# Optimization experiments

Measured on AMD Instinct MI355X. Metric: run time of the kernel, lower is better.

## Reference

```python
import jax, jax.numpy as jnp
import numpy as np

N = 50000          # nodes
E = 800000         # edges (avg degree 16)
H, D = 4, 32       # heads, per-head channels; hidden = H*D = 128
DIMS_IN = [32, 128, 128]


def setup_inputs() -> dict:
    key = jax.random.key(0)
    ks = jax.random.split(key, 40)
    inp = {}
    inp["x"] = jax.random.normal(ks[0], (N, 32), jnp.float32)
    inp["edge_index"] = jax.random.randint(ks[1], (2, E), 0, N, dtype=jnp.int32)
    i = 2
    for l, din in enumerate(DIMS_IN):
        for nm in ["q", "k", "v", "s"]:
            inp[f"W{nm}{l}"] = jax.random.normal(ks[i], (din, H * D), jnp.float32) / np.float32(np.sqrt(din)); i += 1
            inp[f"b{nm}{l}"] = jax.random.normal(ks[i], (H * D,), jnp.float32) * 0.01; i += 1
    inp["Wf"] = jax.random.normal(ks[i], (H * D, 1), jnp.float32) / np.float32(np.sqrt(H * D)); i += 1
    inp["bf"] = jax.random.normal(ks[i], (1,), jnp.float32) * 0.01
    return inp


def _transformer_conv(x, src, dst, Wq, bq, Wk, bk, Wv, bv, Ws, bs):
    """PyG TransformerConv (concat=True, root_weight=True, beta=False, eval mode)."""
    n = x.shape[0]
    q = (x @ Wq + bq).reshape(n, H, D)   # queries at nodes
    k = (x @ Wk + bk).reshape(n, H, D)
    v = (x @ Wv + bv).reshape(n, H, D)
    # per-edge attention score: q at destination, k at source
    s = jnp.einsum("ehd,ehd->eh", q[dst], k[src]) / np.float32(np.sqrt(D))  # [E,H]
    # segment softmax over incoming edges of each destination node
    m = jax.ops.segment_max(s, dst, num_segments=n)          # [N,H]
    e = jnp.exp(s - m[dst])                                  # [E,H]
    den = jax.ops.segment_sum(e, dst, num_segments=n)        # [N,H]
    alpha = e / den[dst]                                     # [E,H]
    agg = jax.ops.segment_sum(alpha[:, :, None] * v[src], dst, num_segments=n)  # [N,H,D]
    return agg.reshape(n, H * D) + (x @ Ws + bs)             # skip connection


def reference(x, edge_index,
              Wq0, bq0, Wk0, bk0, Wv0, bv0, Ws0, bs0,
              Wq1, bq1, Wk1, bk1, Wv1, bv1, Ws1, bs1,
              Wq2, bq2, Wk2, bk2, Wv2, bv2, Ws2, bs2,
              Wf, bf):
    src, dst = edge_index[0], edge_index[1]
    layers = [
        (Wq0, bq0, Wk0, bk0, Wv0, bv0, Ws0, bs0),
        (Wq1, bq1, Wk1, bk1, Wv1, bv1, Ws1, bs1),
        (Wq2, bq2, Wk2, bk2, Wv2, bv2, Ws2, bs2),
    ]
    h = x
    for p in layers:
        h = jax.nn.relu(_transformer_conv(h, src, dst, *p))
    out = jax.nn.sigmoid(h @ Wf + bf)  # [N,1]
    return out
```

## Files before the change

kernel.cpp:

```cpp
#include <hip/hip_runtime.h>
#include <hip/hip_bf16.h>
#include <cstdint>
#include <cstddef>

typedef __attribute__((ext_vector_type(8))) short bf16x8;
typedef __attribute__((ext_vector_type(4))) float f32x4;

__device__ __forceinline__ unsigned short f2bs(float f){
  __hip_bfloat16 h = __float2bfloat16(f);
  return *(unsigned short*)&h;
}
__device__ __forceinline__ float bflo(unsigned int u){ return __uint_as_float(u << 16); }
__device__ __forceinline__ float bfhi(unsigned int u){ return __uint_as_float(u & 0xffff0000u); }

__global__ void zero_int_kernel(int* __restrict__ p, int n){
  int i = blockIdx.x*256 + threadIdx.x;
  if (i < n) p[i] = 0;
}

__global__ void hist_kernel(const int* __restrict__ dst, int E, int* __restrict__ deg){
  int e = blockIdx.x*256 + threadIdx.x;
  if (e < E) atomicAdd(&deg[dst[e]], 1);
}

__global__ __launch_bounds__(1024)
void scanA_kernel(const int* __restrict__ deg, int n, int* __restrict__ rowptr, int* __restrict__ bsums){
  __shared__ int s[1024];
  int t = threadIdx.x;
  int i = blockIdx.x*1024 + t;
  int v = (i < n) ? deg[i] : 0;
  s[t] = v;
  __syncthreads();
  #pragma unroll
  for (int off = 1; off < 1024; off <<= 1){
    int a = (t >= off) ? s[t-off] : 0;
    __syncthreads();
    s[t] += a;
    __syncthreads();
  }
  if (i < n) rowptr[i] = s[t] - v;
  if (t == 1023) bsums[blockIdx.x] = s[1023];
}

__global__ void scanB_kernel(const int* __restrict__ bsums, int nch, int* __restrict__ choff){
  int t = threadIdx.x;
  int v = (t < nch) ? bsums[t] : 0;
  int x = v;
  #pragma unroll
  for (int off = 1; off < 64; off <<= 1){
    int u = __shfl_up(x, off, 64);
    if (t >= off) x += u;
  }
  choff[t] = x - v;
}

__global__ __launch_bounds__(1024)
void scanC_kernel(const int* __restrict__ choff, int n, int* __restrict__ rowptr, int* __restrict__ cursor){
  int i = blockIdx.x*1024 + threadIdx.x;
  if (i < n){
    int r = rowptr[i] + choff[blockIdx.x];
    rowptr[i] = r;
    cursor[i] = r;
  }
}

__global__ void scatter_kernel(const int* __restrict__ src, const int* __restrict__ dst, int E,
                               int* __restrict__ cursor, int* __restrict__ adj){
  int e = blockIdx.x*256 + threadIdx.x;
  if (e < E){
    int pos = atomicAdd(&cursor[dst[e]], 1);
    adj[pos] = src[e];
  }
}

struct PrepArgs {
  const float* w[12];
  unsigned short* o[12];
};

__global__ void transpose_w_kernel(PrepArgs a){
  int m = blockIdx.y;
  int K = (m < 4) ? 32 : 128;
  int halfK = K >> 1;
  int tot = 128 * halfK;
  int e = blockIdx.x*256 + threadIdx.x;
  if (e >= tot) return;
  int n  = e / halfK;
  int k2 = e % halfK;
  const float* W = a.w[m];
  unsigned int lo = __float_as_uint(W[(2*k2)  *128 + n]) >> 16;
  unsigned int hi = __float_as_uint(W[(2*k2+1)*128 + n]) & 0xffff0000u;
  ((unsigned int*)a.o[m])[e] = lo | hi;
}

__global__ void cvt_x_kernel(const float* __restrict__ x, unsigned short* __restrict__ xb, int n2){
  int i = blockIdx.x*256 + threadIdx.x;
  if (i < n2){
    float2 v = ((const float2*)x)[i];
    ((unsigned int*)xb)[i] = (__float_as_uint(v.x) >> 16) | (__float_as_uint(v.y) & 0xffff0000u);
  }
}

template<int DIN>
__global__ __launch_bounds__(256)
void gemm4_mfma(const unsigned short* __restrict__ X, int nn,
                const unsigned short* __restrict__ T0, const unsigned short* __restrict__ T1,
                const unsigned short* __restrict__ T2, const unsigned short* __restrict__ T3,
                const float* __restrict__ b0, const float* __restrict__ b1,
                const float* __restrict__ b2, const float* __restrict__ b3,
                unsigned short* __restrict__ O0, unsigned short* __restrict__ O1,
                unsigned short* __restrict__ O2, unsigned short* __restrict__ O3)
{
  constexpr int KP = DIN + 8;
  __shared__ __align__(16) unsigned short wt[128*KP];
  int t = threadIdx.x;
  int msel = blockIdx.y;
  const unsigned short* WT = (msel==0)?T0:(msel==1)?T1:(msel==2)?T2:T3;
  const float* B = (msel==0)?b0:(msel==1)?b1:(msel==2)?b2:b3;
  unsigned short* O = (msel==0)?O0:(msel==1)?O1:(msel==2)?O2:O3;

  {
    const int NU = 128*DIN/8;
    for (int u = t; u < NU; u += 256){
      uint4 v = ((const uint4*)WT)[u];
      int n = u / (DIN/8), b = u % (DIN/8);
      *(uint4*)&wt[n*KP + b*8] = v;
    }
  }

  int lane = t & 63, wv = t >> 6;
  int m0 = blockIdx.x*64 + wv*16;
  int n16 = lane & 15, quad = lane >> 4;

  bf16x8 af[DIN/32];
  {
    const unsigned short* xrow = X + (size_t)(m0 + n16)*DIN + quad*8;
    #pragma unroll
    for (int s = 0; s < DIN/32; s++) af[s] = *(const bf16x8*)(xrow + s*32);
  }

  __syncthreads();

  f32x4 acc[8];
  #pragma unroll
  for (int c=0;c<8;c++) acc[c] = (f32x4){0.f,0.f,0.f,0.f};

  #pragma unroll
  for (int s = 0; s < DIN/32; s++){
    #pragma unroll
    for (int c = 0; c < 8; c++){
      bf16x8 bf = *(const bf16x8*)&wt[(c*16 + n16)*KP + s*32 + quad*8];
      acc[c] = __builtin_amdgcn_mfma_f32_16x16x32_bf16(af[s], bf, acc[c], 0, 0, 0);
    }
  }

  #pragma unroll
  for (int c = 0; c < 8; c++){
    int col = c*16 + n16;
    float bias = B[col];
    #pragma unroll
    for (int r = 0; r < 4; r++){
      int row = m0 + quad*4 + r;
      if (row < nn) O[(size_t)row*128 + col] = f2bs(acc[c][r] + bias);
    }
  }
}

__global__ __launch_bounds__(256)
void attn_kernel(const unsigned short* __restrict__ q,  const unsigned short* __restrict__ kmat,
                 const unsigned short* __restrict__ vmat, const unsigned short* __restrict__ skip,
                 const int* __restrict__ rowptr, const int* __restrict__ deg,
                 const int* __restrict__ adj, unsigned short* __restrict__ hout, int nn)
{
  int lane = threadIdx.x & 63, wid = threadIdx.x >> 6;
  int n = blockIdx.x*4 + wid;
  if (n >= nn) return;
  const float RS = 0.17677669529663687f;

  unsigned int qu = *(const unsigned int*)(q + (size_t)n*128 + 2*lane);
  float qx = bflo(qu), qy = bfhi(qu);
  int start = rowptr[n], dg = deg[n];
  float m = -INFINITY, l = 0.f, accx = 0.f, accy = 0.f;

  for (int c0 = 0; c0 < dg; c0 += 64){
    int cn = min(64, dg - c0);
    int idx = adj[start + c0 + min(lane, cn-1)];

    for (int g = 0; g < cn; g += 4){
      int gm = cn - g;
      int e1 = min(g+1, cn-1);
      int e2 = min(g+2, cn-1);
      int e3 = min(g+3, cn-1);
      int s0 = __shfl(idx, g , 64);
      int s1 = __shfl(idx, e1, 64);
      int s2 = __shfl(idx, e2, 64);
      int s3 = __shfl(idx, e3, 64);
      unsigned int ku0 = *(const unsigned int*)(kmat + (size_t)s0*128 + 2*lane);
      unsigned int ku1 = *(const unsigned int*)(kmat + (size_t)s1*128 + 2*lane);
      unsigned int ku2 = *(const unsigned int*)(kmat + (size_t)s2*128 + 2*lane);
      unsigned int ku3 = *(const unsigned int*)(kmat + (size_t)s3*128 + 2*lane);
      unsigned int vu0 = *(const unsigned int*)(vmat + (size_t)s0*128 + 2*lane);
      unsigned int vu1 = *(const unsigned int*)(vmat + (size_t)s1*128 + 2*lane);
      unsigned int vu2 = *(const unsigned int*)(vmat + (size_t)s2*128 + 2*lane);
      unsigned int vu3 = *(const unsigned int*)(vmat + (size_t)s3*128 + 2*lane);

      float p0 = qx*bflo(ku0) + qy*bfhi(ku0);
      float p1 = qx*bflo(ku1) + qy*bfhi(ku1);
      float p2 = qx*bflo(ku2) + qy*bfhi(ku2);
      float p3 = qx*bflo(ku3) + qy*bfhi(ku3);
      #pragma unroll
      for (int msk = 1; msk <= 8; msk <<= 1){
        p0 += __shfl_xor(p0, msk, 64);
        p1 += __shfl_xor(p1, msk, 64);
        p2 += __shfl_xor(p2, msk, 64);
        p3 += __shfl_xor(p3, msk, 64);
      }
      float f0 = p0*RS;
      float f1 = (gm > 1) ? p1*RS : -INFINITY;
      float f2 = (gm > 2) ? p2*RS : -INFINITY;
      float f3 = (gm > 3) ? p3*RS : -INFINITY;

      float gmax = fmaxf(fmaxf(f0,f1), fmaxf(f2,f3));
      float nm = fmaxf(m, gmax);
      float r  = __expf(m - nm);
      float w0 = __expf(f0 - nm);
      float w1 = __expf(f1 - nm);
      float w2 = __expf(f2 - nm);
      float w3 = __expf(f3 - nm);
      m = nm;
      l = l*r + ((w0+w1) + (w2+w3));
      accx = accx*r;
      accy = accy*r;
      accx = fmaf(w0, bflo(vu0), accx); accy = fmaf(w0, bfhi(vu0), accy);
      accx = fmaf(w1, bflo(vu1), accx); accy = fmaf(w1, bfhi(vu1), accy);
      accx = fmaf(w2, bflo(vu2), accx); accy = fmaf(w2, bfhi(vu2), accy);
      accx = fmaf(w3, bflo(vu3), accx); accy = fmaf(w3, bfhi(vu3), accy);
    }
  }

  float inv = (l > 0.f) ? 1.f/l : 0.f;
  unsigned int su = *(const unsigned int*)(skip + (size_t)n*128 + 2*lane);
  float ox = fmaxf(fmaf(accx, inv, bflo(su)), 0.f);
  float oy = fmaxf(fmaf(accy, inv, bfhi(su)), 0.f);
  unsigned int pk = (unsigned int)f2bs(ox) | ((unsigned int)f2bs(oy) << 16);
  *(unsigned int*)(hout + (size_t)n*128 + 2*lane) = pk;
}

__global__ __launch_bounds__(256)
void head_kernel(const unsigned short* __restrict__ h, const float* __restrict__ Wf,
                 const float* __restrict__ bfp, float* __restrict__ out, int nn)
{
  int lane = threadIdx.x & 63, wid = threadIdx.x >> 6;
  int n = blockIdx.x*4 + wid;
  if (n >= nn) return;
  unsigned int hu = *(const unsigned int*)(h + (size_t)n*128 + 2*lane);
  float2 wv = *(const float2*)(Wf + 2*lane);
  float p = bflo(hu)*wv.x + bfhi(hu)*wv.y;
  #pragma unroll
  for (int msk = 1; msk <= 32; msk <<= 1) p += __shfl_xor(p, msk, 64);
  if (lane == 0){
    float z = p + bfp[0];
    out[n] = 1.f / (1.f + __expf(-z));
  }
}

extern "C" void kernel_launch(void* const* d_in, const int* in_sizes, int n_in,
                              void* d_out, int out_size, void* d_ws, size_t ws_size,
                              hipStream_t stream) {
  const int N = in_sizes[0] / 32;
  const int E = in_sizes[1] / 2;
  const float* x = (const float*)d_in[0];
  const int* ei  = (const int*)d_in[1];
  const int* src = ei;
  const int* dst = ei + E;
  auto Wp = [&](int i){ return (const float*)d_in[i]; };
  const int NP = N + 64;

  char* p = (char*)d_ws;
  auto alloc = [&](size_t b){ char* r = p; p += (b + 255) & ~(size_t)255; return (void*)r; };
  unsigned short* F0 = (unsigned short*)alloc((size_t)NP*128*2);
  unsigned short* F1 = (unsigned short*)alloc((size_t)NP*128*2);
  unsigned short* Qb = (unsigned short*)alloc((size_t)NP*128*2);
  unsigned short* Kb = (unsigned short*)alloc((size_t)NP*128*2);
  unsigned short* Vb = (unsigned short*)alloc((size_t)NP*128*2);
  unsigned short* xb = (unsigned short*)alloc((size_t)NP*32*2);
  unsigned short* WT[12];
  for (int i = 0; i < 12; i++){
    int K = (i < 4) ? 32 : 128;
    WT[i] = (unsigned short*)alloc((size_t)128*K*2);
  }
  int* deg    = (int*)alloc((size_t)N*4);
  int* rowptr = (int*)alloc((size_t)N*4);
  int* cursor = (int*)alloc((size_t)N*4);
  int* adj    = (int*)alloc((size_t)E*4);
  int* bsums  = (int*)alloc(64*4);
  int* choff  = (int*)alloc(64*4);

  zero_int_kernel<<<(N+255)/256, 256, 0, stream>>>(deg, N);
  hist_kernel<<<(E+255)/256, 256, 0, stream>>>(dst, E, deg);
  int nch = (N + 1023) / 1024;
  scanA_kernel<<<nch, 1024, 0, stream>>>(deg, N, rowptr, bsums);
  scanB_kernel<<<1, 64, 0, stream>>>(bsums, nch, choff);
  scanC_kernel<<<nch, 1024, 0, stream>>>(choff, N, rowptr, cursor);
  scatter_kernel<<<(E+255)/256, 256, 0, stream>>>(src, dst, E, cursor, adj);

  PrepArgs pa;
  const int widx[12] = {2,4,6,8, 10,12,14,16, 18,20,22,24};
  for (int i = 0; i < 12; i++){ pa.w[i] = Wp(widx[i]); pa.o[i] = WT[i]; }
  transpose_w_kernel<<<dim3(32,12), 256, 0, stream>>>(pa);
  cvt_x_kernel<<<(N*16+255)/256, 256, 0, stream>>>(x, xb, N*16);

  dim3 gg((N+63)/64, 4);
  int ab = (N + 3) / 4;
  gemm4_mfma<32><<<gg, 256, 0, stream>>>(xb, N,
      WT[0],WT[1],WT[2],WT[3], Wp(3),Wp(5),Wp(7),Wp(9), Qb,Kb,Vb, F0);
  attn_kernel<<<ab, 256, 0, stream>>>(Qb,Kb,Vb, F0, rowptr,deg,adj, F0, N);
  gemm4_mfma<128><<<gg, 256, 0, stream>>>(F0, N,
      WT[4],WT[5],WT[6],WT[7], Wp(11),Wp(13),Wp(15),Wp(17), Qb,Kb,Vb, F1);
  attn_kernel<<<ab, 256, 0, stream>>>(Qb,Kb,Vb, F1, rowptr,deg,adj, F1, N);
  gemm4_mfma<128><<<gg, 256, 0, stream>>>(F1, N,
      WT[8],WT[9],WT[10],WT[11], Wp(19),Wp(21),Wp(23),Wp(25), Qb,Kb,Vb, F0);
  attn_kernel<<<ab, 256, 0, stream>>>(Qb,Kb,Vb, F0, rowptr,deg,adj, F0, N);
  head_kernel<<<ab, 256, 0, stream>>>(F0, Wp(26), Wp(27), (float*)d_out, N);
}
```

Baseline: 482.6 us.

## Split attention wave into four edge groups with 16B loads and fuse head

```diff
diff --git a/kernel.cpp b/kernel.cpp
--- a/kernel.cpp
+++ b/kernel.cpp
@@ -12,6 +12,10 @@
 }
 __device__ __forceinline__ float bflo(unsigned int u){ return __uint_as_float(u << 16); }
 __device__ __forceinline__ float bfhi(unsigned int u){ return __uint_as_float(u & 0xffff0000u); }
+__device__ __forceinline__ void unp8(uint4 u, float* f){
+  f[0]=bflo(u.x); f[1]=bfhi(u.x); f[2]=bflo(u.y); f[3]=bfhi(u.y);
+  f[4]=bflo(u.z); f[5]=bfhi(u.z); f[6]=bflo(u.w); f[7]=bfhi(u.w);
+}
 
 __global__ void zero_int_kernel(int* __restrict__ p, int n){
   int i = blockIdx.x*256 + threadIdx.x;
@@ -166,101 +170,112 @@
   }
 }
 
+template<bool FINAL>
 __global__ __launch_bounds__(256)
 void attn_kernel(const unsigned short* __restrict__ q,  const unsigned short* __restrict__ kmat,
                  const unsigned short* __restrict__ vmat, const unsigned short* __restrict__ skip,
                  const int* __restrict__ rowptr, const int* __restrict__ deg,
-                 const int* __restrict__ adj, unsigned short* __restrict__ hout, int nn)
+                 const int* __restrict__ adj, unsigned short* __restrict__ hout,
+                 const float* __restrict__ Wf, const float* __restrict__ bfp,
+                 float* __restrict__ out, int nn)
 {
   int lane = threadIdx.x & 63, wid = threadIdx.x >> 6;
   int n = blockIdx.x*4 + wid;
   if (n >= nn) return;
+  int p = lane & 15, g = lane >> 4;
   const float RS = 0.17677669529663687f;
 
-  unsigned int qu = *(const unsigned int*)(q + (size_t)n*128 + 2*lane);
-  float qx = bflo(qu), qy = bfhi(qu);
+  float qf[8];
+  { uint4 qu = *(const uint4*)(q + (size_t)n*128 + p*8); unp8(qu, qf); }
+
   int start = rowptr[n], dg = deg[n];
-  float m = -INFINITY, l = 0.f, accx = 0.f, accy = 0.f;
+  float m = -INFINITY, l = 0.f;
+  float acc[8];
+  #pragma unroll
+  for (int i=0;i<8;i++) acc[i]=0.f;
 
   for (int c0 = 0; c0 < dg; c0 += 64){
     int cn = min(64, dg - c0);
     int idx = adj[start + c0 + min(lane, cn-1)];
-
-    for (int g = 0; g < cn; g += 4){
-      int gm = cn - g;
-      int e1 = min(g+1, cn-1);
-      int e2 = min(g+2, cn-1);
-      int e3 = min(g+3, cn-1);
-      int s0 = __shfl(idx, g , 64);
-      int s1 = __shfl(idx, e1, 64);
-      int s2 = __shfl(idx, e2, 64);
-      int s3 = __shfl(idx, e3, 64);
-      unsigned int ku0 = *(const unsigned int*)(kmat + (size_t)s0*128 + 2*lane);
-      unsigned int ku1 = *(const unsigned int*)(kmat + (size_t)s1*128 + 2*lane);
-      unsigned int ku2 = *(const unsigned int*)(kmat + (size_t)s2*128 + 2*lane);
-      unsigned int ku3 = *(const unsigned int*)(kmat + (size_t)s3*128 + 2*lane);
-      unsigned int vu0 = *(const unsigned int*)(vmat + (size_t)s0*128 + 2*lane);
-      unsigned int vu1 = *(const unsigned int*)(vmat + (size_t)s1*128 + 2*lane);
-      unsigned int vu2 = *(const unsigned int*)(vmat + (size_t)s2*128 + 2*lane);
-      unsigned int vu3 = *(const unsigned int*)(vmat + (size_t)s3*128 + 2*lane);
-
-      float p0 = qx*bflo(ku0) + qy*bfhi(ku0);
-      float p1 = qx*bflo(ku1) + qy*bfhi(ku1);
-      float p2 = qx*bflo(ku2) + qy*bfhi(ku2);
-      float p3 = qx*bflo(ku3) + qy*bfhi(ku3);
+    int nit = (cn + 3) >> 2;
+
+    bool val = g < cn;
+    int s0 = __shfl(idx, min(g, cn-1), 64);
+    uint4 ku = *(const uint4*)(kmat + (size_t)s0*128 + p*8);
+    uint4 vu = *(const uint4*)(vmat + (size_t)s0*128 + p*8);
+
+    for (int it = 0; it < nit; ++it){
+      int j2 = (it+1)*4 + g;
+      bool val2 = j2 < cn;
+      int s2 = __shfl(idx, min(j2, cn-1), 64);
+      uint4 ku2 = {0,0,0,0}, vu2 = {0,0,0,0};
+      if (it + 1 < nit){
+        ku2 = *(const uint4*)(kmat + (size_t)s2*128 + p*8);
+        vu2 = *(const uint4*)(vmat + (size_t)s2*128 + p*8);
+      }
+      float kf[8]; unp8(ku, kf);
+      float d = qf[0]*kf[0];
       #pragma unroll
-      for (int msk = 1; msk <= 8; msk <<= 1){
-        p0 += __shfl_xor(p0, msk, 64);
-        p1 += __shfl_xor(p1, msk, 64);
-        p2 += __shfl_xor(p2, msk, 64);
-        p3 += __shfl_xor(p3, msk, 64);
-      }
-      float f0 = p0*RS;
-      float f1 = (gm > 1) ? p1*RS : -INFINITY;
-      float f2 = (gm > 2) ? p2*RS : -INFINITY;
-      float f3 = (gm > 3) ? p3*RS : -INFINITY;
-
-      float gmax = fmaxf(fmaxf(f0,f1), fmaxf(f2,f3));
-      float nm = fmaxf(m, gmax);
-      float r  = __expf(m - nm);
-      float w0 = __expf(f0 - nm);
-      float w1 = __expf(f1 - nm);
-      float w2 = __expf(f2 - nm);
-      float w3 = __expf(f3 - nm);
+      for (int i=1;i<8;i++) d = fmaf(qf[i], kf[i], d);
+      d += __shfl_xor(d, 1, 64);
+      d += __shfl_xor(d, 2, 64);
+      float f = val ? d*RS : -INFINITY;
+      float nm = fmaxf(m, f);
+      float r = __expf(fmaxf(m - nm, -80.f));
+      float w = __expf(fmaxf(f - nm, -80.f));
       m = nm;
-      l = l*r + ((w0+w1) + (w2+w3));
-      accx = accx*r;
-      accy = accy*r;
-      accx = fmaf(w0, bflo(vu0), accx); accy = fmaf(w0, bfhi(vu0), accy);
-      accx = fmaf(w1, bflo(vu1), accx); accy = fmaf(w1, bfhi(vu1), accy);
-      accx = fmaf(w2, bflo(vu2), accx); accy = fmaf(w2, bfhi(vu2), accy);
-      accx = fmaf(w3, bflo(vu3), accx); accy = fmaf(w3, bfhi(vu3), accy);
-    }
-  }
-
-  float inv = (l > 0.f) ? 1.f/l : 0.f;
-  unsigned int su = *(const unsigned int*)(skip + (size_t)n*128 + 2*lane);
-  float ox = fmaxf(fmaf(accx, inv, bflo(su)), 0.f);
-  float oy = fmaxf(fmaf(accy, inv, bfhi(su)), 0.f);
-  unsigned int pk = (unsigned int)f2bs(ox) | ((unsigned int)f2bs(oy) << 16);
-  *(unsigned int*)(hout + (size_t)n*128 + 2*lane) = pk;
-}
-
-__global__ __launch_bounds__(256)
-void head_kernel(const unsigned short* __restrict__ h, const float* __restrict__ Wf,
-                 const float* __restrict__ bfp, float* __restrict__ out, int nn)
-{
-  int lane = threadIdx.x & 63, wid = threadIdx.x >> 6;
-  int n = blockIdx.x*4 + wid;
-  if (n >= nn) return;
-  unsigned int hu = *(const unsigned int*)(h + (size_t)n*128 + 2*lane);
-  float2 wv = *(const float2*)(Wf + 2*lane);
-  float p = bflo(hu)*wv.x + bfhi(hu)*wv.y;
-  #pragma unroll
-  for (int msk = 1; msk <= 32; msk <<= 1) p += __shfl_xor(p, msk, 64);
-  if (lane == 0){
-    float z = p + bfp[0];
-    out[n] = 1.f / (1.f + __expf(-z));
+      l = l*r + w;
+      float vf[8]; unp8(vu, vf);
+      #pragma unroll
+      for (int i=0;i<8;i++) acc[i] = fmaf(w, vf[i], acc[i]*r);
+      ku = ku2; vu = vu2; val = val2;
+    }
+  }
+
+  float m1 = fmaxf(m, __shfl_xor(m, 16, 64));
+  float M  = fmaxf(m1, __shfl_xor(m1, 32, 64));
+  float sc = __expf(fmaxf(m - M, -80.f));
+  float lp = l * sc;
+  float l1 = lp + __shfl_xor(lp, 16, 64);
+  float L  = l1 + __shfl_xor(l1, 32, 64);
+  #pragma unroll
+  for (int i=0;i<8;i++){
+    float a = acc[i]*sc;
+    a += __shfl_xor(a, 16, 64);
+    a += __shfl_xor(a, 32, 64);
+    acc[i] = a;
+  }
+  float inv = (L > 0.f) ? 1.f/L : 0.f;
+  float sk[8];
+  { uint4 su = *(const uint4*)(skip + (size_t)n*128 + p*8); unp8(su, sk); }
+  float o[8];
+  #pragma unroll
+  for (int i=0;i<8;i++) o[i] = fmaxf(fmaf(acc[i], inv, sk[i]), 0.f);
+
+  if constexpr (!FINAL){
+    if (g == 0){
+      uint4 st;
+      st.x = (unsigned)f2bs(o[0]) | ((unsigned)f2bs(o[1])<<16);
+      st.y = (unsigned)f2bs(o[2]) | ((unsigned)f2bs(o[3])<<16);
+      st.z = (unsigned)f2bs(o[4]) | ((unsigned)f2bs(o[5])<<16);
+      st.w = (unsigned)f2bs(o[6]) | ((unsigned)f2bs(o[7])<<16);
+      *(uint4*)(hout + (size_t)n*128 + p*8) = st;
+    }
+  } else {
+    float4 w0 = *(const float4*)(Wf + p*8);
+    float4 w1 = *(const float4*)(Wf + p*8 + 4);
+    float pd = o[0]*w0.x;
+    pd = fmaf(o[1], w0.y, pd); pd = fmaf(o[2], w0.z, pd); pd = fmaf(o[3], w0.w, pd);
+    pd = fmaf(o[4], w1.x, pd); pd = fmaf(o[5], w1.y, pd);
+    pd = fmaf(o[6], w1.z, pd); pd = fmaf(o[7], w1.w, pd);
+    pd += __shfl_xor(pd, 1, 64);
+    pd += __shfl_xor(pd, 2, 64);
+    pd += __shfl_xor(pd, 4, 64);
+    pd += __shfl_xor(pd, 8, 64);
+    if (lane == 0){
+      float z = pd + bfp[0];
+      out[n] = 1.f / (1.f + __expf(-z));
+    }
   }
 }
 
@@ -314,12 +329,14 @@
   int ab = (N + 3) / 4;
   gemm4_mfma<32><<<gg, 256, 0, stream>>>(xb, N,
       WT[0],WT[1],WT[2],WT[3], Wp(3),Wp(5),Wp(7),Wp(9), Qb,Kb,Vb, F0);
-  attn_kernel<<<ab, 256, 0, stream>>>(Qb,Kb,Vb, F0, rowptr,deg,adj, F0, N);
+  attn_kernel<false><<<ab, 256, 0, stream>>>(Qb,Kb,Vb, F0, rowptr,deg,adj, F0,
+      nullptr, nullptr, nullptr, N);
   gemm4_mfma<128><<<gg, 256, 0, stream>>>(F0, N,
       WT[4],WT[5],WT[6],WT[7], Wp(11),Wp(13),Wp(15),Wp(17), Qb,Kb,Vb, F1);
-  attn_kernel<<<ab, 256, 0, stream>>>(Qb,Kb,Vb, F1, rowptr,deg,adj, F1, N);
+  attn_kernel<false><<<ab, 256, 0, stream>>>(Qb,Kb,Vb, F1, rowptr,deg,adj, F1,
+      nullptr, nullptr, nullptr, N);
   gemm4_mfma<128><<<gg, 256, 0, stream>>>(F1, N,
       WT[8],WT[9],WT[10],WT[11], Wp(19),Wp(21),Wp(23),Wp(25), Qb,Kb,Vb, F0);
-  attn_kernel<<<ab, 256, 0, stream>>>(Qb,Kb,Vb, F0, rowptr,deg,adj, F0, N);
-  head_kernel<<<ab, 256, 0, stream>>>(F0, Wp(26), Wp(27), (float*)d_out, N);
-}
+  attn_kernel<true><<<ab, 256, 0, stream>>>(Qb,Kb,Vb, F0, rowptr,deg,adj, nullptr,
+      Wp(26), Wp(27), (float*)d_out, N);
+}
```

After: 472.7 us. -2.0%, faster.
